# Kernel optimization log

Hardware: AMD Instinct MI355X
Metric: run time of the kernel (lower is better)

Reference implementation:

```python
import jax, jax.numpy as jnp
import numpy as np

N, E = 50000, 800000
INF, ONF, HNF = 64, 64, 128
EPS = 1e-8


def qmul(p, q):
    # roma XYZW Hamilton product
    px, py, pz, pw = p[:, 0], p[:, 1], p[:, 2], p[:, 3]
    qx, qy, qz, qw = q[:, 0], q[:, 1], q[:, 2], q[:, 3]
    return jnp.stack([
        pw * qx + px * qw + py * qz - pz * qy,
        pw * qy - px * qz + py * qw + pz * qx,
        pw * qz + px * qy - py * qx + pz * qw,
        pw * qw - px * qx - py * qy - pz * qz,
    ], axis=1)


def qinv(q):
    conj = jnp.concatenate([-q[:, :3], q[:, 3:]], axis=1)
    return conj / jnp.sum(q * q, axis=1, keepdims=True)


def rot_apply(q, v):
    # rotate v by unit quaternion q (XYZW)
    qv, w = q[:, :3], q[:, 3:4]
    t = 2.0 * jnp.cross(qv, v)
    return v + w * t + jnp.cross(qv, t)


def quat_exponential(im):
    r = jnp.linalg.norm(im, axis=1, keepdims=True)
    u = im / r
    return jnp.concatenate([u * jnp.sin(r), jnp.cos(r)], axis=1)


def seg_sum(data, ids, n):
    return jax.ops.segment_sum(data, ids, num_segments=n)


def seg_mean(data, ids, n):
    s = seg_sum(data, ids, n)
    c = seg_sum(jnp.ones_like(data), ids, n)
    return s / jnp.maximum(c, 1.0)


def setup_inputs() -> dict:
    key = jax.random.key(0)
    ks = jax.random.split(key, 24)
    h = jax.random.normal(ks[0], (N, INF), jnp.float32)
    coord = jax.random.normal(ks[1], (N, 3), jnp.float32)
    q = jax.random.normal(ks[2], (N, 4), jnp.float32)
    quat = q / jnp.linalg.norm(q, axis=1, keepdims=True)
    edge_index = jax.random.randint(ks[3], (2, E), 0, N)

    def lin(k, fi, fo, scale=None):
        s = (1.0 / np.sqrt(fi)) if scale is None else scale
        return jax.random.uniform(k, (fi, fo), jnp.float32, -s, s)

    ein = 2 * INF + 8  # source, target, radial(1), quat_prod(4), unit_vecs(3)
    params = dict(
        We1=lin(ks[4], ein, HNF), be1=jnp.zeros((HNF,), jnp.float32),
        We2=lin(ks[5], HNF, HNF), be2=jnp.zeros((HNF,), jnp.float32),
        Wn1=lin(ks[6], HNF + INF, HNF), bn1=jnp.zeros((HNF,), jnp.float32),
        Wn2=lin(ks[7], HNF, ONF), bn2=jnp.zeros((ONF,), jnp.float32),
        Wc1=lin(ks[8], HNF, HNF), bc1=jnp.zeros((HNF,), jnp.float32),
        wc2=lin(ks[9], HNF, 1, scale=0.001),  # xavier gain 0.001, no bias
        Wq1=lin(ks[10], HNF, HNF), bq1=jnp.zeros((HNF,), jnp.float32),
        Wq2=lin(ks[11], HNF, 3), bq2=jnp.zeros((3,), jnp.float32),
    )
    return dict(h=h, edge_index=edge_index, coord=coord, quat=quat, **params)


def reference(h, edge_index, coord, quat,
              We1, be1, We2, be2, Wn1, bn1, Wn2, bn2,
              Wc1, bc1, wc2, Wq1, bq1, Wq2, bq2):
    silu = jax.nn.silu
    row, col = edge_index[0], edge_index[1]

    # invariants
    coord_diff = coord[row] - coord[col]                       # [E,3]
    qi = qinv(quat)
    quat_prod = qmul(qi[row], quat[col])                       # [E,4]
    radial = jnp.sum(coord_diff ** 2, axis=1, keepdims=True)   # [E,1]
    norm = jnp.sqrt(radial) + EPS
    unit_vecs = -rot_apply(qi[row], coord_diff / norm)         # [E,3]

    # edge model
    ein = jnp.concatenate([h[row], h[col], radial, quat_prod, unit_vecs], axis=1)
    edge_feat = silu(silu(ein @ We1 + be1) @ We2 + be2)        # [E,HNF]

    # coord model (mean agg)
    trans = coord_diff * (silu(edge_feat @ Wc1 + bc1) @ wc2)   # [E,3]
    coord = coord + seg_mean(trans, row, N)

    # quat model (mean agg)
    tan_vecs = silu(edge_feat @ Wq1 + bq1) @ Wq2 + bq2         # [E,3]
    rots = quat_exponential(seg_mean(tan_vecs, row, N))
    quat = qmul(quat, rots)

    # node model (sum agg), residual
    agg = seg_sum(edge_feat, row, N)
    nin = jnp.concatenate([h, agg], axis=1)
    h = h + (silu(nin @ Wn1 + bn1) @ Wn2 + bn2)
    return (h, coord, quat)
```

## Files before the change

kernel.cpp:

```cpp
#include <hip/hip_runtime.h>
#include <hip/hip_bf16.h>
#include <math.h>


#define N_NODES 50000
#define N_EDGES 800000
#define ASTR 172
#define NSTR 204

typedef __attribute__((ext_vector_type(4))) float f32x4;
typedef __attribute__((ext_vector_type(8))) short bf16x8;
typedef __attribute__((ext_vector_type(4))) unsigned short u16x4;
typedef __attribute__((ext_vector_type(8))) unsigned short u16x8;

static __device__ __forceinline__ unsigned short f2bf(float f) {
  return __builtin_bit_cast(unsigned short, __float2bfloat16(f));
}
static __device__ __forceinline__ float bf2f(unsigned short s) {
  unsigned int u = ((unsigned int)s) << 16;
  return __builtin_bit_cast(float, u);
}
static __device__ __forceinline__ float silu_f(float x) {
  return x * __builtin_amdgcn_rcpf(1.0f + __expf(-x));
}
static __device__ __forceinline__ void atomic_pk_add_bf16(unsigned int* addr,
                                                          float lo, float hi) {
  const unsigned int pk = ((unsigned int)f2bf(hi) << 16) | (unsigned int)f2bf(lo);
  asm volatile("global_atomic_pk_add_bf16 %0, %1, off"
               :: "v"((unsigned long long)(uintptr_t)addr), "v"(pk)
               : "memory");
}

static __device__ __forceinline__ void swz_do(const float* __restrict__ src,
                                              unsigned short* __restrict__ dst,
                                              int K, int NOUT, int NCT, int idx) {
  int lane = idx & 63, blk = idx >> 6;
  int ct = blk % NCT, kt = blk / NCT;
  int col = ct * 16 + (lane & 15);
  int kb = kt * 32 + (lane >> 4) * 8;
  u16x8 o;
  #pragma unroll
  for (int j = 0; j < 8; ++j) {
    int k = kb + j;
    o[j] = (k < K) ? f2bf(src[(size_t)k * NOUT + col]) : (unsigned short)0;
  }
  *(u16x8*)(dst + (size_t)idx * 8) = o;
}

__global__ __launch_bounds__(256) void prep1_kernel(
    const float* __restrict__ We1, const float* __restrict__ We2,
    const float* __restrict__ Wc1, const float* __restrict__ Wq1,
    const float* __restrict__ Wn1, const float* __restrict__ Wn2,
    const float* __restrict__ h,
    unsigned short* __restrict__ We1b, unsigned short* __restrict__ We2b,
    unsigned short* __restrict__ Wc1b, unsigned short* __restrict__ Wq1b,
    unsigned short* __restrict__ Wn1b, unsigned short* __restrict__ Wn2b,
    unsigned short* __restrict__ hb, uint4* __restrict__ zbase,
    const int* __restrict__ ei, int* __restrict__ cursor)
{
  const int b = blockIdx.x, t = threadIdx.x;
  if (b < 50) {
    if (b < 10)       swz_do(We1, We1b, 136, 128, 8, b*256 + t);
    else if (b < 18)  swz_do(We2, We2b, 128, 128, 8, (b-10)*256 + t);
    else if (b < 26)  swz_do(Wc1, Wc1b, 128, 128, 8, (b-18)*256 + t);
    else if (b < 34)  swz_do(Wq1, Wq1b, 128, 128, 8, (b-26)*256 + t);
    else if (b < 46) { int i = (b-34)*256 + t; if (i < 3072) swz_do(Wn1, Wn1b, 192, 128, 8, i); }
    else              swz_do(Wn2, Wn2b, 128, 64, 4, (b-46)*256 + t);
    return;
  }
  if (b < 1613) {
    const int i8 = (b - 50) * 2048 + t * 8;
    if (i8 < N_NODES * 64) {
      f32x4 v0 = *(const f32x4*)(h + i8);
      f32x4 v1 = *(const f32x4*)(h + i8 + 4);
      u16x8 o;
      #pragma unroll
      for (int i = 0; i < 4; ++i) { o[i] = f2bf(v0[i]); o[i+4] = f2bf(v1[i]); }
      *(u16x8*)(hb + i8) = o;
    }
    return;
  }
  if (b < 5031) {
    const int i = (b - 1613) * 256 + t;
    if (i < 875000) { uint4 z; z.x = z.y = z.z = z.w = 0u; zbase[i] = z; }
    return;
  }
  const int e = (b - 5031) * 256 + t;
  if (e < N_EDGES) atomicAdd(&cursor[ei[e]], 1);
}

__global__ void scan_kernel(int* __restrict__ cursor) {
  __shared__ int s[1024];
  const int t = threadIdx.x;
  const int C = 49;
  const int base = t * C;
  int sum = 0;
  for (int i = 0; i < C; ++i) {
    int n = base + i;
    if (n < N_NODES) sum += cursor[n];
  }
  s[t] = sum;
  __syncthreads();
  for (int d = 1; d < 1024; d <<= 1) {
    int v = (t >= d) ? s[t - d] : 0;
    __syncthreads();
    s[t] += v;
    __syncthreads();
  }
  int run = s[t] - sum;
  for (int i = 0; i < C; ++i) {
    int n = base + i;
    if (n < N_NODES) {
      int d = cursor[n];
      cursor[n] = run;
      run += d;
    }
  }
}

__global__ void scatter_kernel(const int* __restrict__ ei, int* __restrict__ cursor,
                               int2* __restrict__ rc2) {
  int e = blockIdx.x * blockDim.x + threadIdx.x;
  if (e < N_EDGES) {
    int r = ei[e];
    int pos = atomicAdd(&cursor[r], 1);
    int2 v; v.x = r; v.y = ei[N_EDGES + e];
    rc2[pos] = v;
  }
}

template <int KT, int NCT>
static __device__ __forceinline__ void mmW2(const unsigned short* __restrict__ a0,
                                            const unsigned short* __restrict__ a1,
                                            int lk,
                                            const unsigned short* __restrict__ Wb,
                                            const float* __restrict__ bias,
                                            int lane, f32x4* acc0, f32x4* acc1) {
  #pragma unroll
  for (int ct = 0; ct < NCT; ++ct) {
    const f32x4 b = *(const f32x4*)&bias[ct*16 + lk*4];
    acc0[ct] = b; acc1[ct] = b;
  }
  __builtin_amdgcn_s_setprio(1);
  #pragma unroll
  for (int kt = 0; kt < KT; ++kt) {
    bf16x8 x0 = *(const bf16x8*)(a0 + kt*32 + lk*8);
    bf16x8 x1 = *(const bf16x8*)(a1 + kt*32 + lk*8);
    const u16x8* bb = (const u16x8*)Wb + (size_t)(kt*NCT)*64 + lane;
    #pragma unroll
    for (int ct = 0; ct < NCT; ++ct) {
      bf16x8 w = *(const bf16x8*)(bb + (size_t)ct*64);
      acc0[ct] = __builtin_amdgcn_mfma_f32_16x16x32_bf16(w, x0, acc0[ct], 0, 0, 0);
      acc1[ct] = __builtin_amdgcn_mfma_f32_16x16x32_bf16(w, x1, acc1[ct], 0, 0, 0);
    }
  }
  __builtin_amdgcn_s_setprio(0);
}

__global__ __launch_bounds__(128, 3) void edge_kernel(
    const unsigned short* __restrict__ hb,
    const float* __restrict__ coord, const float* __restrict__ quat,
    const int2* __restrict__ rc2,
    const unsigned short* __restrict__ We1b, const unsigned short* __restrict__ We2b,
    const unsigned short* __restrict__ Wc1b, const unsigned short* __restrict__ Wq1b,
    const float* __restrict__ be1, const float* __restrict__ be2,
    const float* __restrict__ bc1, const float* __restrict__ wc2,
    const float* __restrict__ bq1, const float* __restrict__ Wq2,
    const float* __restrict__ bq2,
    unsigned int* __restrict__ agg32, float* __restrict__ transS,
    float* __restrict__ tanS)
{
  __shared__ __align__(16) unsigned short AF[64 * ASTR];

  const int tid = threadIdx.x;
  const int wv = tid >> 6, lane = tid & 63;
  const int lr = lane & 15, lk = lane >> 4;
  const int row0 = wv*32 + lr, row1 = row0 + 16;

  const int xcd = blockIdx.x & 7, idx = blockIdx.x >> 3;
  const int q = 1562, rem = 4;
  const int bid = (xcd < rem ? xcd*(q+1) : rem*(q+1) + (xcd-rem)*q) + idx;
  const int e0 = bid * 64;

  const int2 p0v = rc2[e0 + row0];
  const int2 p1v = rc2[e0 + row1];
  const int r0 = p0v.x, c0 = p0v.y, r1 = p1v.x, c1 = p1v.y;

  {
    const unsigned short* hs0 = hb + (size_t)(lk < 2 ? r0 : c0) * 64 + (lk & 1) * 32;
    const unsigned short* hs1 = hb + (size_t)(lk < 2 ? r1 : c1) * 64 + (lk & 1) * 32;
    const int cb = lk * 32;
    #pragma unroll
    for (int j = 0; j < 32; j += 4) {
      *(u16x4*)&AF[row0*ASTR + cb + j] = *(const u16x4*)(hs0 + j);
      *(u16x4*)&AF[row1*ASTR + cb + j] = *(const u16x4*)(hs1 + j);
    }
  }
  const float cdx0 = coord[r0*3+0] - coord[c0*3+0];
  const float cdy0 = coord[r0*3+1] - coord[c0*3+1];
  const float cdz0 = coord[r0*3+2] - coord[c0*3+2];
  const float cdx1 = coord[r1*3+0] - coord[c1*3+0];
  const float cdy1 = coord[r1*3+1] - coord[c1*3+1];
  const float cdz1 = coord[r1*3+2] - coord[c1*3+2];
  if (lk < 2) {
    const int gr = lk ? r1 : r0, gc = lk ? c1 : c0, grow = lk ? row1 : row0;
    const float gx = lk ? cdx1 : cdx0, gy = lk ? cdy1 : cdy0, gz = lk ? cdz1 : cdz0;
    const float radial = gx*gx + gy*gy + gz*gz;
    const float nrm = sqrtf(radial) + 1e-8f;
    const f32x4 qr4 = *(const f32x4*)&quat[gr*4];
    const f32x4 qc4 = *(const f32x4*)&quat[gc*4];
    const float qix = -qr4[0], qiy = -qr4[1], qiz = -qr4[2], qiw = qr4[3];
    const float qcx = qc4[0], qcy = qc4[1], qcz = qc4[2], qcw = qc4[3];
    const float qpx = qiw*qcx + qix*qcw + qiy*qcz - qiz*qcy;
    const float qpy = qiw*qcy - qix*qcz + qiy*qcw + qiz*qcx;
    const float qpz = qiw*qcz + qix*qcy - qiy*qcx + qiz*qcw;
    const float qpw = qiw*qcw - qix*qcx - qiy*qcy - qiz*qcz;
    const float rinv = __builtin_amdgcn_rcpf(nrm);
    const float vx = gx*rinv, vy = gy*rinv, vz = gz*rinv;
    const float tx = 2.f*(qiy*vz - qiz*vy);
    const float ty = 2.f*(qiz*vx - qix*vz);
    const float tz = 2.f*(qix*vy - qiy*vx);
    const float ux = -(vx + qiw*tx + (qiy*tz - qiz*ty));
    const float uy = -(vy + qiw*ty + (qiz*tx - qix*tz));
    const float uz = -(vz + qiw*tz + (qix*ty - qiy*tx));
    u16x4 f0, f1;
    f0[0] = f2bf(radial); f0[1] = f2bf(qpx); f0[2] = f2bf(qpy); f0[3] = f2bf(qpz);
    f1[0] = f2bf(qpw);    f1[1] = f2bf(ux);  f1[2] = f2bf(uy);  f1[3] = f2bf(uz);
    *(u16x4*)&AF[grow*ASTR + 128] = f0;
    *(u16x4*)&AF[grow*ASTR + 132] = f1;
    const u16x4 z4 = {0, 0, 0, 0};
    #pragma unroll
    for (int j = 136; j < 160; j += 4) *(u16x4*)&AF[grow*ASTR + j] = z4;
  }

  f32x4 acc0[8], acc1[8];

  mmW2<5,8>(AF + row0*ASTR, AF + row1*ASTR, lk, We1b, be1, lane, acc0, acc1);
  #pragma unroll
  for (int ct = 0; ct < 8; ++ct) {
    const int ocb = ct*16 + lk*4;
    u16x4 k0, k1;
    #pragma unroll
    for (int i = 0; i < 4; ++i) {
      k0[i] = f2bf(silu_f(acc0[ct][i]));
      k1[i] = f2bf(silu_f(acc1[ct][i]));
    }
    *(u16x4*)&AF[row0*ASTR + ocb] = k0;
    *(u16x4*)&AF[row1*ASTR + ocb] = k1;
  }

  mmW2<4,8>(AF + row0*ASTR, AF + row1*ASTR, lk, We2b, be2, lane, acc0, acc1);
  #pragma unroll
  for (int ct = 0; ct < 8; ++ct) {
    const int ocb = ct*16 + lk*4;
    u16x4 k0, k1;
    #pragma unroll
    for (int i = 0; i < 4; ++i) {
      k0[i] = f2bf(silu_f(acc0[ct][i]));
      k1[i] = f2bf(silu_f(acc1[ct][i]));
    }
    *(u16x4*)&AF[row0*ASTR + ocb] = k0;
    *(u16x4*)&AF[row1*ASTR + ocb] = k1;
  }

  float pcs0 = 0.f, pcs1 = 0.f;
  mmW2<4,8>(AF + row0*ASTR, AF + row1*ASTR, lk, Wc1b, bc1, lane, acc0, acc1);
  #pragma unroll
  for (int ct = 0; ct < 8; ++ct) {
    const int ocb = ct*16 + lk*4;
    const f32x4 w4 = *(const f32x4*)&wc2[ocb];
    #pragma unroll
    for (int i = 0; i < 4; ++i) {
      pcs0 += silu_f(acc0[ct][i]) * w4[i];
      pcs1 += silu_f(acc1[ct][i]) * w4[i];
    }
  }
  pcs0 += __shfl_xor(pcs0, 16);  pcs0 += __shfl_xor(pcs0, 32);
  pcs1 += __shfl_xor(pcs1, 16);  pcs1 += __shfl_xor(pcs1, 32);

  float p00 = 0.f, p10 = 0.f, p20 = 0.f;
  float p01 = 0.f, p11 = 0.f, p21 = 0.f;
  mmW2<4,8>(AF + row0*ASTR, AF + row1*ASTR, lk, Wq1b, bq1, lane, acc0, acc1);
  #pragma unroll
  for (int ct = 0; ct < 8; ++ct) {
    const int ocb = ct*16 + lk*4;
    const float* wq = &Wq2[ocb*3];
    const f32x4 qa = *(const f32x4*)(wq);
    const f32x4 qb = *(const f32x4*)(wq + 4);
    const f32x4 qc = *(const f32x4*)(wq + 8);
    {
      const float v0 = silu_f(acc0[ct][0]);
      const float v1 = silu_f(acc0[ct][1]);
      const float v2 = silu_f(acc0[ct][2]);
      const float v3 = silu_f(acc0[ct][3]);
      p00 += v0*qa[0] + v1*qa[3] + v2*qb[2] + v3*qc[1];
      p10 += v0*qa[1] + v1*qb[0] + v2*qb[3] + v3*qc[2];
      p20 += v0*qa[2] + v1*qb[1] + v2*qc[0] + v3*qc[3];
    }
    {
      const float v0 = silu_f(acc1[ct][0]);
      const float v1 = silu_f(acc1[ct][1]);
      const float v2 = silu_f(acc1[ct][2]);
      const float v3 = silu_f(acc1[ct][3]);
      p01 += v0*qa[0] + v1*qa[3] + v2*qb[2] + v3*qc[1];
      p11 += v0*qa[1] + v1*qb[0] + v2*qb[3] + v3*qc[2];
      p21 += v0*qa[2] + v1*qb[1] + v2*qc[0] + v3*qc[3];
    }
  }
  p00 += __shfl_xor(p00, 16);  p00 += __shfl_xor(p00, 32);
  p10 += __shfl_xor(p10, 16);  p10 += __shfl_xor(p10, 32);
  p20 += __shfl_xor(p20, 16);  p20 += __shfl_xor(p20, 32);
  p01 += __shfl_xor(p01, 16);  p01 += __shfl_xor(p01, 32);
  p11 += __shfl_xor(p11, 16);  p11 += __shfl_xor(p11, 32);
  p21 += __shfl_xor(p21, 16);  p21 += __shfl_xor(p21, 32);

  if (lk < 3) {
    #pragma unroll
    for (int g = 0; g < 2; ++g) {
      const int rg = g ? r1 : r0;
      const int rUp = __shfl_up(rg, 1, 16);
      const int rDn = __shfl_down(rg, 1, 16);
      const bool head = (lr == 0) || (rUp != rg);
      const bool tail = (lr == 15) || (rDn != rg);
      const float cdj = (lk == 0) ? (g ? cdx1 : cdx0)
                      : (lk == 1) ? (g ? cdy1 : cdy0) : (g ? cdz1 : cdz0);
      const float pj  = (lk == 0) ? (g ? p01 : p00)
                      : (lk == 1) ? (g ? p11 : p10) : (g ? p21 : p20);
      float v1 = cdj * (g ? pcs1 : pcs0);
      float v2 = pj + bq2[lk];
      int f = head ? 1 : 0;
      #pragma unroll
      for (int d = 1; d < 16; d <<= 1) {
        const float o1 = __shfl_up(v1, d, 16);
        const float o2 = __shfl_up(v2, d, 16);
        const int   of = __shfl_up(f,  d, 16);
        if (lr >= d) {
          if (!f) { v1 += o1; v2 += o2; }
          f |= of;
        }
      }
      if (tail) {
        atomicAdd(&transS[rg*3 + lk], v1);
        atomicAdd(&tanS[rg*3 + lk], v2);
      }
    }
  }

  {
    float rl_ = 0.f, rh_ = 0.f;
    int prev = __builtin_amdgcn_readlane(r0, 0);
    #pragma unroll
    for (int k2 = 0; k2 < 32; ++k2) {
      const int rr = (k2 < 16) ? __builtin_amdgcn_readlane(r0, k2)
                               : __builtin_amdgcn_readlane(r1, k2 - 16);
      if (rr != prev) {
        atomic_pk_add_bf16(&agg32[(size_t)prev*64 + lane], rl_, rh_);
        rl_ = 0.f; rh_ = 0.f; prev = rr;
      }
      const unsigned int u = *(const unsigned int*)&AF[(wv*32 + k2)*ASTR + 2*lane];
      rl_ += bf2f((unsigned short)(u & 0xffffu));
      rh_ += bf2f((unsigned short)(u >> 16));
    }
    atomic_pk_add_bf16(&agg32[(size_t)prev*64 + lane], rl_, rh_);
  }
}

__global__ __launch_bounds__(256, 4) void node_kernel(
    const float* __restrict__ h, const unsigned short* __restrict__ hb,
    const float* __restrict__ coord, const float* __restrict__ quat,
    const unsigned short* __restrict__ aggb, const float* __restrict__ transS,
    const float* __restrict__ tanS, const int* __restrict__ cursor,
    const unsigned short* __restrict__ Wn1b, const unsigned short* __restrict__ Wn2b,
    const float* __restrict__ bn1, const float* __restrict__ bn2,
    float* __restrict__ out_h, float* __restrict__ out_c, float* __restrict__ out_q)
{
  __shared__ unsigned short A_[64][NSTR];
  const int tid = threadIdx.x;
  const int n0 = blockIdx.x * 64;

  {
    const int row = tid >> 2, sub = tid & 3;
    const int n = n0 + row;
    if (n < N_NODES) {
      if (sub < 2) {
        const unsigned short* hp = hb + (size_t)n*64 + sub*32;
        #pragma unroll
        for (int j = 0; j < 32; j += 4)
          *(u16x4*)&A_[row][sub*32 + j] = *(const u16x4*)(hp + j);
      } else {
        const unsigned short* ap = aggb + (size_t)n*128 + (sub - 2)*64;
        #pragma unroll
        for (int j = 0; j < 64; j += 8)
          *(u16x8*)&A_[row][64 + (sub - 2)*64 + j] = *(const u16x8*)(ap + j);
      }
    } else {
      const u16x4 z4 = {0, 0, 0, 0};
      if (sub < 2) {
        #pragma unroll
        for (int j = 0; j < 32; j += 4) *(u16x4*)&A_[row][sub*32 + j] = z4;
      } else {
        #pragma unroll
        for (int j = 0; j < 64; j += 4) *(u16x4*)&A_[row][64 + (sub - 2)*64 + j] = z4;
      }
    }
  }
  __syncthreads();

  const int wv = tid >> 6, lane = tid & 63;
  const int lr = lane & 15, lk = lane >> 4;
  const int nrow = wv*16 + lr;
  f32x4 acc[8];

  {
    #pragma unroll
    for (int ct = 0; ct < 8; ++ct)
      acc[ct] = *(const f32x4*)&bn1[ct*16 + lk*4];
    #pragma unroll
    for (int kt = 0; kt < 6; ++kt) {
      bf16x8 act = *(const bf16x8*)&A_[nrow][kt*32 + lk*8];
      const u16x8* bb = (const u16x8*)Wn1b + (size_t)(kt*8)*64 + lane;
      #pragma unroll
      for (int ct = 0; ct < 8; ++ct) {
        bf16x8 w = *(const bf16x8*)(bb + (size_t)ct*64);
        acc[ct] = __builtin_amdgcn_mfma_f32_16x16x32_bf16(w, act, acc[ct], 0, 0, 0);
      }
    }
  }
  #pragma unroll
  for (int ct = 0; ct < 8; ++ct) {
    const int ocb = ct*16 + lk*4;
    u16x4 pk;
    #pragma unroll
    for (int i = 0; i < 4; ++i) pk[i] = f2bf(silu_f(acc[ct][i]));
    *(u16x4*)&A_[nrow][ocb] = pk;
  }

  f32x4 acc2[4];
  {
    #pragma unroll
    for (int ct = 0; ct < 4; ++ct)
      acc2[ct] = *(const f32x4*)&bn2[ct*16 + lk*4];
    #pragma unroll
    for (int kt = 0; kt < 4; ++kt) {
      bf16x8 act = *(const bf16x8*)&A_[nrow][kt*32 + lk*8];
      const u16x8* bb = (const u16x8*)Wn2b + (size_t)(kt*4)*64 + lane;
      #pragma unroll
      for (int ct = 0; ct < 4; ++ct) {
        bf16x8 w = *(const bf16x8*)(bb + (size_t)ct*64);
        acc2[ct] = __builtin_amdgcn_mfma_f32_16x16x32_bf16(w, act, acc2[ct], 0, 0, 0);
      }
    }
  }
  const int n = n0 + nrow;
  if (n < N_NODES) {
    #pragma unroll
    for (int ct = 0; ct < 4; ++ct) {
      const int ocb = ct*16 + lk*4;
      const f32x4 h4 = *(const f32x4*)&h[(size_t)n*64 + ocb];
      f32x4 o;
      #pragma unroll
      for (int i = 0; i < 4; ++i) o[i] = h4[i] + acc2[ct][i];
      *(f32x4*)&out_h[(size_t)n*64 + ocb] = o;
    }
  }

  if (tid < 64) {
    const int nn = n0 + tid;
    if (nn < N_NODES) {
      const int deg = cursor[nn] - (nn ? cursor[nn-1] : 0);
      const float inv = 1.0f / fmaxf((float)deg, 1.0f);
      out_c[nn*3+0] = coord[nn*3+0] + transS[nn*3+0]*inv;
      out_c[nn*3+1] = coord[nn*3+1] + transS[nn*3+1]*inv;
      out_c[nn*3+2] = coord[nn*3+2] + transS[nn*3+2]*inv;
      const float ix = tanS[nn*3+0]*inv, iy = tanS[nn*3+1]*inv, iz = tanS[nn*3+2]*inv;
      const float rr = sqrtf(ix*ix + iy*iy + iz*iz);
      const float s = sinf(rr) / rr;
      const float rx = ix*s, ry = iy*s, rz = iz*s, rw = cosf(rr);
      const float px = quat[nn*4+0], py = quat[nn*4+1], pz = quat[nn*4+2], pw = quat[nn*4+3];
      out_q[nn*4+0] = pw*rx + px*rw + py*rz - pz*ry;
      out_q[nn*4+1] = pw*ry - px*rz + py*rw + pz*rx;
      out_q[nn*4+2] = pw*rz + px*ry - py*rx + pz*rw;
      out_q[nn*4+3] = pw*rw - px*rx - py*ry - pz*rz;
    }
  }
}

extern "C" void kernel_launch(void* const* d_in, const int* in_sizes, int n_in,
                              void* d_out, int out_size, void* d_ws, size_t ws_size,
                              hipStream_t stream) {
  (void)in_sizes; (void)n_in; (void)out_size; (void)ws_size;
  const float* h     = (const float*)d_in[0];
  const int*   ei    = (const int*)d_in[1];
  const float* coord = (const float*)d_in[2];
  const float* quat  = (const float*)d_in[3];
  const float* We1 = (const float*)d_in[4];  const float* be1 = (const float*)d_in[5];
  const float* We2 = (const float*)d_in[6];  const float* be2 = (const float*)d_in[7];
  const float* Wn1 = (const float*)d_in[8];  const float* bn1 = (const float*)d_in[9];
  const float* Wn2 = (const float*)d_in[10]; const float* bn2 = (const float*)d_in[11];
  const float* Wc1 = (const float*)d_in[12]; const float* bc1 = (const float*)d_in[13];
  const float* wc2 = (const float*)d_in[14];
  const float* Wq1 = (const float*)d_in[15]; const float* bq1 = (const float*)d_in[16];
  const float* Wq2 = (const float*)d_in[17]; const float* bq2 = (const float*)d_in[18];

  char* ws = (char*)d_ws;
  unsigned int* agg32  = (unsigned int*)(ws);
  unsigned short* aggb = (unsigned short*)(ws);
  float* transS = (float*)(ws + 12800000);
  float* tanS   = (float*)(ws + 13400000);
  int*   cursor = (int*)  (ws + 14200000);
  int2*  rc2    = (int2*) (ws + 14600064);
  unsigned short* We1b = (unsigned short*)(ws + 21000064);
  unsigned short* We2b = We1b + 5*8*64*8;
  unsigned short* Wc1b = We2b + 4*8*64*8;
  unsigned short* Wq1b = Wc1b + 4*8*64*8;
  unsigned short* Wn1b = Wq1b + 4*8*64*8;
  unsigned short* Wn2b = Wn1b + 6*8*64*8;
  unsigned short* hb   = (unsigned short*)(ws + 21204864);

  hipMemsetAsync(cursor, 0, 200000, stream);
  prep1_kernel<<<8156, 256, 0, stream>>>(
      We1, We2, Wc1, Wq1, Wn1, Wn2, h,
      We1b, We2b, Wc1b, Wq1b, Wn1b, Wn2b, hb, (uint4*)ws, ei, cursor);
  scan_kernel<<<1, 1024, 0, stream>>>(cursor);
  scatter_kernel<<<(N_EDGES + 255)/256, 256, 0, stream>>>(ei, cursor, rc2);

  edge_kernel<<<N_EDGES/64, 128, 0, stream>>>(
      hb, coord, quat, rc2, We1b, We2b, Wc1b, Wq1b,
      be1, be2, bc1, wc2, bq1, Wq2, bq2, agg32, transS, tanS);

  float* out_h = (float*)d_out;
  float* out_c = out_h + (size_t)N_NODES*64;
  float* out_q = out_c + (size_t)N_NODES*3;
  node_kernel<<<(N_NODES + 63)/64, 256, 0, stream>>>(
      h, hb, coord, quat, aggb, transS, tanS, cursor, Wn1b, Wn2b, bn1, bn2,
      out_h, out_c, out_q);
}
```

Before: 459.1 us.

## Process 64 edges per single wave to reuse weight fragments across four row groups

The edge kernel moves from two waves of 32 edges each to one 64-lane wave that handles all 64 edges of the block as four 16-row groups. Each weight fragment loaded from global memory now feeds four MFMAs instead of two, which halves weight traffic per edge. In exchange the accumulator state doubles to 32 f32x4 registers per lane, so register pressure rises and occupancy may drop. Workgroups now hold only one wave while still using the same amount of LDS, and the launch bounds change to match.

```diff
diff --git a/kernel.cpp b/kernel.cpp
--- a/kernel.cpp
+++ b/kernel.cpp
@@ -130,34 +130,38 @@
 }
 
 template <int KT, int NCT>
-static __device__ __forceinline__ void mmW2(const unsigned short* __restrict__ a0,
-                                            const unsigned short* __restrict__ a1,
+static __device__ __forceinline__ void mmW4(const unsigned short* __restrict__ abase,
                                             int lk,
                                             const unsigned short* __restrict__ Wb,
                                             const float* __restrict__ bias,
-                                            int lane, f32x4* acc0, f32x4* acc1) {
+                                            int lane, f32x4 acc[4][8]) {
   #pragma unroll
   for (int ct = 0; ct < NCT; ++ct) {
     const f32x4 b = *(const f32x4*)&bias[ct*16 + lk*4];
-    acc0[ct] = b; acc1[ct] = b;
+    #pragma unroll
+    for (int g = 0; g < 4; ++g) acc[g][ct] = b;
   }
   __builtin_amdgcn_s_setprio(1);
   #pragma unroll
   for (int kt = 0; kt < KT; ++kt) {
-    bf16x8 x0 = *(const bf16x8*)(a0 + kt*32 + lk*8);
-    bf16x8 x1 = *(const bf16x8*)(a1 + kt*32 + lk*8);
+    bf16x8 x0 = *(const bf16x8*)(abase + 0*16*ASTR + kt*32 + lk*8);
+    bf16x8 x1 = *(const bf16x8*)(abase + 1*16*ASTR + kt*32 + lk*8);
+    bf16x8 x2 = *(const bf16x8*)(abase + 2*16*ASTR + kt*32 + lk*8);
+    bf16x8 x3 = *(const bf16x8*)(abase + 3*16*ASTR + kt*32 + lk*8);
     const u16x8* bb = (const u16x8*)Wb + (size_t)(kt*NCT)*64 + lane;
     #pragma unroll
     for (int ct = 0; ct < NCT; ++ct) {
       bf16x8 w = *(const bf16x8*)(bb + (size_t)ct*64);
-      acc0[ct] = __builtin_amdgcn_mfma_f32_16x16x32_bf16(w, x0, acc0[ct], 0, 0, 0);
-      acc1[ct] = __builtin_amdgcn_mfma_f32_16x16x32_bf16(w, x1, acc1[ct], 0, 0, 0);
+      acc[0][ct] = __builtin_amdgcn_mfma_f32_16x16x32_bf16(w, x0, acc[0][ct], 0, 0, 0);
+      acc[1][ct] = __builtin_amdgcn_mfma_f32_16x16x32_bf16(w, x1, acc[1][ct], 0, 0, 0);
+      acc[2][ct] = __builtin_amdgcn_mfma_f32_16x16x32_bf16(w, x2, acc[2][ct], 0, 0, 0);
+      acc[3][ct] = __builtin_amdgcn_mfma_f32_16x16x32_bf16(w, x3, acc[3][ct], 0, 0, 0);
     }
   }
   __builtin_amdgcn_s_setprio(0);
 }
 
-__global__ __launch_bounds__(128, 3) void edge_kernel(
+__global__ __launch_bounds__(64, 2) void edge_kernel(
     const unsigned short* __restrict__ hb,
     const float* __restrict__ coord, const float* __restrict__ quat,
     const int2* __restrict__ rc2,
@@ -172,39 +176,45 @@
 {
   __shared__ __align__(16) unsigned short AF[64 * ASTR];
 
-  const int tid = threadIdx.x;
-  const int wv = tid >> 6, lane = tid & 63;
+  const int lane = threadIdx.x;
   const int lr = lane & 15, lk = lane >> 4;
-  const int row0 = wv*32 + lr, row1 = row0 + 16;
 
   const int xcd = blockIdx.x & 7, idx = blockIdx.x >> 3;
   const int q = 1562, rem = 4;
   const int bid = (xcd < rem ? xcd*(q+1) : rem*(q+1) + (xcd-rem)*q) + idx;
   const int e0 = bid * 64;
 
-  const int2 p0v = rc2[e0 + row0];
-  const int2 p1v = rc2[e0 + row1];
-  const int r0 = p0v.x, c0 = p0v.y, r1 = p1v.x, c1 = p1v.y;
+  int r[4], c[4];
+  float cdx[4], cdy[4], cdz[4];
+  #pragma unroll
+  for (int g = 0; g < 4; ++g) {
+    const int2 pv = rc2[e0 + g*16 + lr];
+    r[g] = pv.x; c[g] = pv.y;
+  }
+  #pragma unroll
+  for (int g = 0; g < 4; ++g) {
+    cdx[g] = coord[r[g]*3+0] - coord[c[g]*3+0];
+    cdy[g] = coord[r[g]*3+1] - coord[c[g]*3+1];
+    cdz[g] = coord[r[g]*3+2] - coord[c[g]*3+2];
+  }
+
+  #pragma unroll
+  for (int g = 0; g < 4; ++g) {
+    const int node = (lk < 2) ? r[g] : c[g];
+    const unsigned short* hs = hb + (size_t)node * 64 + (lk & 1) * 32;
+    const int dst = (g*16 + lr)*ASTR + lk*32;
+    #pragma unroll
+    for (int j = 0; j < 32; j += 4)
+      *(u16x4*)&AF[dst + j] = *(const u16x4*)(hs + j);
+  }
 
   {
-    const unsigned short* hs0 = hb + (size_t)(lk < 2 ? r0 : c0) * 64 + (lk & 1) * 32;
-    const unsigned short* hs1 = hb + (size_t)(lk < 2 ? r1 : c1) * 64 + (lk & 1) * 32;
-    const int cb = lk * 32;
-    #pragma unroll
-    for (int j = 0; j < 32; j += 4) {
-      *(u16x4*)&AF[row0*ASTR + cb + j] = *(const u16x4*)(hs0 + j);
-      *(u16x4*)&AF[row1*ASTR + cb + j] = *(const u16x4*)(hs1 + j);
-    }
-  }
-  const float cdx0 = coord[r0*3+0] - coord[c0*3+0];
-  const float cdy0 = coord[r0*3+1] - coord[c0*3+1];
-  const float cdz0 = coord[r0*3+2] - coord[c0*3+2];
-  const float cdx1 = coord[r1*3+0] - coord[c1*3+0];
-  const float cdy1 = coord[r1*3+1] - coord[c1*3+1];
-  const float cdz1 = coord[r1*3+2] - coord[c1*3+2];
-  if (lk < 2) {
-    const int gr = lk ? r1 : r0, gc = lk ? c1 : c0, grow = lk ? row1 : row0;
-    const float gx = lk ? cdx1 : cdx0, gy = lk ? cdy1 : cdy0, gz = lk ? cdz1 : cdz0;
+    const int gr = (lk == 0) ? r[0] : (lk == 1) ? r[1] : (lk == 2) ? r[2] : r[3];
+    const int gc = (lk == 0) ? c[0] : (lk == 1) ? c[1] : (lk == 2) ? c[2] : c[3];
+    const float gx = (lk == 0) ? cdx[0] : (lk == 1) ? cdx[1] : (lk == 2) ? cdx[2] : cdx[3];
+    const float gy = (lk == 0) ? cdy[0] : (lk == 1) ? cdy[1] : (lk == 2) ? cdy[2] : cdy[3];
+    const float gz = (lk == 0) ? cdz[0] : (lk == 1) ? cdz[1] : (lk == 2) ? cdz[2] : cdz[3];
+    const int grow = lane;
     const float radial = gx*gx + gy*gy + gz*gz;
     const float nrm = sqrtf(radial) + 1e-8f;
     const f32x4 qr4 = *(const f32x4*)&quat[gr*4];
@@ -233,100 +243,89 @@
     for (int j = 136; j < 160; j += 4) *(u16x4*)&AF[grow*ASTR + j] = z4;
   }
 
-  f32x4 acc0[8], acc1[8];
-
-  mmW2<5,8>(AF + row0*ASTR, AF + row1*ASTR, lk, We1b, be1, lane, acc0, acc1);
+  f32x4 acc[4][8];
+  const unsigned short* abase = AF + lr*ASTR;
+
+  mmW4<5,8>(abase, lk, We1b, be1, lane, acc);
+  #pragma unroll
+  for (int g = 0; g < 4; ++g) {
+    #pragma unroll
+    for (int ct = 0; ct < 8; ++ct) {
+      const int ocb = ct*16 + lk*4;
+      u16x4 k0;
+      #pragma unroll
+      for (int i = 0; i < 4; ++i) k0[i] = f2bf(silu_f(acc[g][ct][i]));
+      *(u16x4*)&AF[(g*16 + lr)*ASTR + ocb] = k0;
+    }
+  }
+
+  mmW4<4,8>(abase, lk, We2b, be2, lane, acc);
+  #pragma unroll
+  for (int g = 0; g < 4; ++g) {
+    #pragma unroll
+    for (int ct = 0; ct < 8; ++ct) {
+      const int ocb = ct*16 + lk*4;
+      u16x4 k0;
+      #pragma unroll
+      for (int i = 0; i < 4; ++i) k0[i] = f2bf(silu_f(acc[g][ct][i]));
+      *(u16x4*)&AF[(g*16 + lr)*ASTR + ocb] = k0;
+    }
+  }
+
+  float pcs[4] = {0.f, 0.f, 0.f, 0.f};
+  mmW4<4,8>(abase, lk, Wc1b, bc1, lane, acc);
   #pragma unroll
   for (int ct = 0; ct < 8; ++ct) {
-    const int ocb = ct*16 + lk*4;
-    u16x4 k0, k1;
-    #pragma unroll
-    for (int i = 0; i < 4; ++i) {
-      k0[i] = f2bf(silu_f(acc0[ct][i]));
-      k1[i] = f2bf(silu_f(acc1[ct][i]));
-    }
-    *(u16x4*)&AF[row0*ASTR + ocb] = k0;
-    *(u16x4*)&AF[row1*ASTR + ocb] = k1;
-  }
-
-  mmW2<4,8>(AF + row0*ASTR, AF + row1*ASTR, lk, We2b, be2, lane, acc0, acc1);
+    const f32x4 w4 = *(const f32x4*)&wc2[ct*16 + lk*4];
+    #pragma unroll
+    for (int g = 0; g < 4; ++g) {
+      #pragma unroll
+      for (int i = 0; i < 4; ++i) pcs[g] += silu_f(acc[g][ct][i]) * w4[i];
+    }
+  }
+  #pragma unroll
+  for (int g = 0; g < 4; ++g) {
+    pcs[g] += __shfl_xor(pcs[g], 16);
+    pcs[g] += __shfl_xor(pcs[g], 32);
+  }
+
+  float p0[4] = {0.f,0.f,0.f,0.f}, p1[4] = {0.f,0.f,0.f,0.f}, p2[4] = {0.f,0.f,0.f,0.f};
+  mmW4<4,8>(abase, lk, Wq1b, bq1, lane, acc);
   #pragma unroll
   for (int ct = 0; ct < 8; ++ct) {
-    const int ocb = ct*16 + lk*4;
-    u16x4 k0, k1;
-    #pragma unroll
-    for (int i = 0; i < 4; ++i) {
-      k0[i] = f2bf(silu_f(acc0[ct][i]));
-      k1[i] = f2bf(silu_f(acc1[ct][i]));
-    }
-    *(u16x4*)&AF[row0*ASTR + ocb] = k0;
-    *(u16x4*)&AF[row1*ASTR + ocb] = k1;
-  }
-
-  float pcs0 = 0.f, pcs1 = 0.f;
-  mmW2<4,8>(AF + row0*ASTR, AF + row1*ASTR, lk, Wc1b, bc1, lane, acc0, acc1);
-  #pragma unroll
-  for (int ct = 0; ct < 8; ++ct) {
-    const int ocb = ct*16 + lk*4;
-    const f32x4 w4 = *(const f32x4*)&wc2[ocb];
-    #pragma unroll
-    for (int i = 0; i < 4; ++i) {
-      pcs0 += silu_f(acc0[ct][i]) * w4[i];
-      pcs1 += silu_f(acc1[ct][i]) * w4[i];
-    }
-  }
-  pcs0 += __shfl_xor(pcs0, 16);  pcs0 += __shfl_xor(pcs0, 32);
-  pcs1 += __shfl_xor(pcs1, 16);  pcs1 += __shfl_xor(pcs1, 32);
-
-  float p00 = 0.f, p10 = 0.f, p20 = 0.f;
-  float p01 = 0.f, p11 = 0.f, p21 = 0.f;
-  mmW2<4,8>(AF + row0*ASTR, AF + row1*ASTR, lk, Wq1b, bq1, lane, acc0, acc1);
-  #pragma unroll
-  for (int ct = 0; ct < 8; ++ct) {
-    const int ocb = ct*16 + lk*4;
-    const float* wq = &Wq2[ocb*3];
+    const float* wq = &Wq2[(ct*16 + lk*4)*3];
     const f32x4 qa = *(const f32x4*)(wq);
     const f32x4 qb = *(const f32x4*)(wq + 4);
     const f32x4 qc = *(const f32x4*)(wq + 8);
-    {
-      const float v0 = silu_f(acc0[ct][0]);
-      const float v1 = silu_f(acc0[ct][1]);
-      const float v2 = silu_f(acc0[ct][2]);
-      const float v3 = silu_f(acc0[ct][3]);
-      p00 += v0*qa[0] + v1*qa[3] + v2*qb[2] + v3*qc[1];
-      p10 += v0*qa[1] + v1*qb[0] + v2*qb[3] + v3*qc[2];
-      p20 += v0*qa[2] + v1*qb[1] + v2*qc[0] + v3*qc[3];
-    }
-    {
-      const float v0 = silu_f(acc1[ct][0]);
-      const float v1 = silu_f(acc1[ct][1]);
-      const float v2 = silu_f(acc1[ct][2]);
-      const float v3 = silu_f(acc1[ct][3]);
-      p01 += v0*qa[0] + v1*qa[3] + v2*qb[2] + v3*qc[1];
-      p11 += v0*qa[1] + v1*qb[0] + v2*qb[3] + v3*qc[2];
-      p21 += v0*qa[2] + v1*qb[1] + v2*qc[0] + v3*qc[3];
-    }
-  }
-  p00 += __shfl_xor(p00, 16);  p00 += __shfl_xor(p00, 32);
-  p10 += __shfl_xor(p10, 16);  p10 += __shfl_xor(p10, 32);
-  p20 += __shfl_xor(p20, 16);  p20 += __shfl_xor(p20, 32);
-  p01 += __shfl_xor(p01, 16);  p01 += __shfl_xor(p01, 32);
-  p11 += __shfl_xor(p11, 16);  p11 += __shfl_xor(p11, 32);
-  p21 += __shfl_xor(p21, 16);  p21 += __shfl_xor(p21, 32);
+    #pragma unroll
+    for (int g = 0; g < 4; ++g) {
+      const float v0 = silu_f(acc[g][ct][0]);
+      const float v1 = silu_f(acc[g][ct][1]);
+      const float v2 = silu_f(acc[g][ct][2]);
+      const float v3 = silu_f(acc[g][ct][3]);
+      p0[g] += v0*qa[0] + v1*qa[3] + v2*qb[2] + v3*qc[1];
+      p1[g] += v0*qa[1] + v1*qb[0] + v2*qb[3] + v3*qc[2];
+      p2[g] += v0*qa[2] + v1*qb[1] + v2*qc[0] + v3*qc[3];
+    }
+  }
+  #pragma unroll
+  for (int g = 0; g < 4; ++g) {
+    p0[g] += __shfl_xor(p0[g], 16);  p0[g] += __shfl_xor(p0[g], 32);
+    p1[g] += __shfl_xor(p1[g], 16);  p1[g] += __shfl_xor(p1[g], 32);
+    p2[g] += __shfl_xor(p2[g], 16);  p2[g] += __shfl_xor(p2[g], 32);
+  }
 
   if (lk < 3) {
     #pragma unroll
-    for (int g = 0; g < 2; ++g) {
-      const int rg = g ? r1 : r0;
+    for (int g = 0; g < 4; ++g) {
+      const int rg = r[g];
       const int rUp = __shfl_up(rg, 1, 16);
       const int rDn = __shfl_down(rg, 1, 16);
       const bool head = (lr == 0) || (rUp != rg);
       const bool tail = (lr == 15) || (rDn != rg);
-      const float cdj = (lk == 0) ? (g ? cdx1 : cdx0)
-                      : (lk == 1) ? (g ? cdy1 : cdy0) : (g ? cdz1 : cdz0);
-      const float pj  = (lk == 0) ? (g ? p01 : p00)
-                      : (lk == 1) ? (g ? p11 : p10) : (g ? p21 : p20);
-      float v1 = cdj * (g ? pcs1 : pcs0);
+      const float cdj = (lk == 0) ? cdx[g] : (lk == 1) ? cdy[g] : cdz[g];
+      const float pj  = (lk == 0) ? p0[g]  : (lk == 1) ? p1[g]  : p2[g];
+      float v1 = cdj * pcs[g];
       float v2 = pj + bq2[lk];
       int f = head ? 1 : 0;
       #pragma unroll
@@ -348,18 +347,19 @@
 
   {
     float rl_ = 0.f, rh_ = 0.f;
-    int prev = __builtin_amdgcn_readlane(r0, 0);
-    #pragma unroll
-    for (int k2 = 0; k2 < 32; ++k2) {
-      const int rr = (k2 < 16) ? __builtin_amdgcn_readlane(r0, k2)
-                               : __builtin_amdgcn_readlane(r1, k2 - 16);
-      if (rr != prev) {
-        atomic_pk_add_bf16(&agg32[(size_t)prev*64 + lane], rl_, rh_);
-        rl_ = 0.f; rh_ = 0.f; prev = rr;
-      }
-      const unsigned int u = *(const unsigned int*)&AF[(wv*32 + k2)*ASTR + 2*lane];
-      rl_ += bf2f((unsigned short)(u & 0xffffu));
-      rh_ += bf2f((unsigned short)(u >> 16));
+    int prev = __builtin_amdgcn_readlane(r[0], 0);
+    #pragma unroll
+    for (int g = 0; g < 4; ++g) {
+      for (int k = 0; k < 16; ++k) {
+        const int rr = __builtin_amdgcn_readlane(r[g], k);
+        if (rr != prev) {
+          atomic_pk_add_bf16(&agg32[(size_t)prev*64 + lane], rl_, rh_);
+          rl_ = 0.f; rh_ = 0.f; prev = rr;
+        }
+        const unsigned int u = *(const unsigned int*)&AF[(g*16 + k)*ASTR + 2*lane];
+        rl_ += bf2f((unsigned short)(u & 0xffffu));
+        rh_ += bf2f((unsigned short)(u >> 16));
+      }
     }
     atomic_pk_add_bf16(&agg32[(size_t)prev*64 + lane], rl_, rh_);
   }
@@ -524,7 +524,7 @@
   scan_kernel<<<1, 1024, 0, stream>>>(cursor);
   scatter_kernel<<<(N_EDGES + 255)/256, 256, 0, stream>>>(ei, cursor, rc2);
 
-  edge_kernel<<<N_EDGES/64, 128, 0, stream>>>(
+  edge_kernel<<<N_EDGES/64, 64, 0, stream>>>(
       hb, coord, quat, rc2, We1b, We2b, Wc1b, Wq1b,
       be1, be2, bc1, wc2, bq1, Wq2, bq2, agg32, transS, tanS);
 
```

Measured after the change: 480.7 us. 4.7% more time.
